# Performance work log

Measured on AMD Instinct MI355X. Metric: run time of the kernel, lower is better.

The kernel has to match this reference:

```python
import jax, jax.numpy as jnp
import numpy as np
import math

N = 512
H = 512
L = 16384
R_MIN, R_MAX, MAX_PHASE = 0.0, 1.0, 6.283


def setup_inputs() -> dict:
    key = jax.random.key(0)
    ks = jax.random.split(key, 8)
    u1 = jax.random.uniform(ks[0], (N,))
    u2 = jax.random.uniform(ks[1], (N,))
    nu_log = jnp.log(-0.5 * jnp.log(u1 * (R_MAX ** 2 - R_MIN ** 2) + R_MIN ** 2))
    theta_log = jnp.log(u2 * MAX_PHASE)
    B_re = jax.random.normal(ks[2], (N, H)) / math.sqrt(2 * H)
    B_im = jax.random.normal(ks[3], (N, H)) / math.sqrt(2 * H)
    C_re = jax.random.normal(ks[4], (H, N)) / math.sqrt(N)
    C_im = jax.random.normal(ks[5], (H, N)) / math.sqrt(N)
    D = jax.random.normal(ks[6], (H,))
    diag_lambda = jnp.exp(-jnp.exp(nu_log) + 1j * jnp.exp(theta_log))
    gamma_log = jnp.log(jnp.sqrt(1.0 - jnp.abs(diag_lambda) ** 2))
    x = jax.random.normal(ks[7], (L, H), dtype=jnp.float32)
    # state is Lambda's multiplier in the original code; ones => standard LRU
    state_re = jnp.ones((N,), dtype=jnp.float32)
    state_im = jnp.zeros((N,), dtype=jnp.float32)
    return {"x": x, "state_re": state_re, "state_im": state_im,
            "nu_log": nu_log, "theta_log": theta_log, "gamma_log": gamma_log,
            "B_re": B_re, "B_im": B_im, "C_re": C_re, "C_im": C_im, "D": D}


def _binop(ei, ej):
    a_i, bu_i = ei
    a_j, bu_j = ej
    return (a_j * a_i, a_j * bu_i + bu_j)


def reference(x, state_re, state_im, nu_log, theta_log, gamma_log,
              B_re, B_im, C_re, C_im, D):
    Lambda = jnp.exp(-jnp.exp(nu_log) + 1j * jnp.exp(theta_log))  # (N,) c64
    # NOTE: original uses exp(i*gamma_log) (a phase), faithful here
    exp_gamma = jnp.exp(1j * gamma_log.astype(jnp.complex64))      # (N,)
    B = (B_re + 1j * B_im) * exp_gamma[:, None]                    # (N,H)
    C = C_re + 1j * C_im                                           # (H,N)
    state = state_re + 1j * state_im                               # (N,)
    a0 = Lambda * state                                            # (N,)
    a_elems = jnp.broadcast_to(a0, (x.shape[0], a0.shape[0]))      # (L,N)
    xc = x.astype(jnp.complex64)                                   # (L,H)
    Bu = xc @ B.T                                                  # (L,N)
    _, inner_states = jax.lax.associative_scan(_binop, (a_elems, Bu))
    y = jnp.real(inner_states @ C.T) + D[None, :] * x              # (L,H)
    return y
```

## Files before the change

kernel.cpp:

```cpp
#include <hip/hip_runtime.h>
#include <hip/hip_bf16.h>
#include <cstdint>

#define L_SEQ 16384
#define NST   512
#define HDIM  512
#define CH    512
#define CT    32

typedef __attribute__((ext_vector_type(8))) short short8;
typedef __attribute__((ext_vector_type(4))) float f32x4;

static __device__ __forceinline__ ushort f2bf(float f) {
  union { float f; unsigned int u; } v; v.f = f;
  unsigned int r = v.u + 0x7fffu + ((v.u >> 16) & 1u);
  return (ushort)(r >> 16);
}
static __device__ __forceinline__ float bf2f(ushort u) {
  union { unsigned int u; float f; } v; v.u = ((unsigned int)u) << 16;
  return v.f;
}

static __device__ __forceinline__ void mfma_16x16x32_bf16(f32x4& d, short8 a, short8 b) {
  asm("v_mfma_f32_16x16x32_bf16 %0, %1, %2, %0" : "+v"(d) : "v"(a), "v"(b));
}

static __device__ __forceinline__ void gload_lds16(const ushort* g, ushort* l) {
  __builtin_amdgcn_global_load_lds((__attribute__((address_space(1))) void*)(g),
                                   (__attribute__((address_space(3))) void*)(l),
                                   16, 0, 0);
}

__global__ __launch_bounds__(256) void setup_kernel(
    const float* __restrict__ st_re, const float* __restrict__ st_im,
    const float* __restrict__ nu_log, const float* __restrict__ theta_log,
    const float* __restrict__ gamma_log,
    const float* __restrict__ B_re, const float* __restrict__ B_im,
    const float* __restrict__ C_re, const float* __restrict__ C_im,
    float2* __restrict__ lam, float2* __restrict__ lamT,
    ushort* __restrict__ W1, ushort* __restrict__ W2)
{
  int bid = blockIdx.x, tid = threadIdx.x;
  if (bid < 1024) {
    int idx = bid * 256 + tid;
    int n = idx >> 9, h = idx & 511;
    float g = gamma_log[n];
    float sg, cg; sincosf(g, &sg, &cg);
    float br = B_re[idx], bi = B_im[idx];
    W1[(size_t)n * 512 + h]         = f2bf(br * cg - bi * sg);
    W1[(size_t)(n + 512) * 512 + h] = f2bf(br * sg + bi * cg);
  } else if (bid < 2048) {
    int idx = (bid - 1024) * 256 + tid;
    int hh = idx >> 9, n = idx & 511;
    W2[(size_t)hh * 1024 + n]       = f2bf(C_re[idx]);
    W2[(size_t)hh * 1024 + 512 + n] = f2bf(-C_im[idx]);
  } else {
    int n = (bid - 2048) * 256 + tid;
    float nu  = expf(nu_log[n]);
    float th  = expf(theta_log[n]);
    float mag = expf(-nu);
    float sth, cth; sincosf(th, &sth, &cth);
    float lr = mag * cth, li = mag * sth;
    float sr = st_re[n], si = st_im[n];
    float ar = lr * sr - li * si;
    float ai = lr * si + li * sr;
    lam[n] = make_float2(ar, ai);
    float pr = ar, pi = ai;
#pragma unroll
    for (int i = 0; i < 5; ++i) {
      float nr = pr * pr - pi * pi;
      float ni = 2.f * pr * pi;
      pr = nr; pi = ni;
    }
    lamT[n] = make_float2(pr, pi);
  }
}

__global__ __launch_bounds__(256) void castX(const float* __restrict__ X,
                                             ushort* __restrict__ xb)
{
  size_t i = ((size_t)blockIdx.x * 256 + threadIdx.x) * 8;
#pragma unroll
  for (int j = 0; j < 8; j += 4) {
    float4 v = *(const float4*)(X + i + j);
    ushort4 o;
    o.x = f2bf(v.x); o.y = f2bf(v.y); o.z = f2bf(v.z); o.w = f2bf(v.w);
    *(ushort4*)(xb + i + j) = o;
  }
}

template <int BM, int BN, int WMW, int WNW, int EPI>
__global__ __launch_bounds__(WMW * WNW * 64, 2)
void gemm_p(const ushort* __restrict__ A, const ushort* __restrict__ Bm,
            ushort* __restrict__ Cb, float* __restrict__ Cf,
            const float* __restrict__ Dv, const float* __restrict__ X,
            int M, int Ncols, int K)
{
  constexpr int THREADS = WMW * WNW * 64;
  constexpr int FM = BM / (WMW * 16);
  constexpr int FN = BN / (WNW * 16);
  constexpr int SLOT = (BM + BN) * 32;
  constexpr int GR = (BM + BN) * 4;
  constexpr int LPT = GR / THREADS;
  static_assert(LPT == 4, "vmcnt immediates assume 4 loads/thread/tile");
  __shared__ __align__(16) ushort lds[4 * SLOT];

  const int t = threadIdx.x, lane = t & 63, w = t >> 6;
  const int wr = w / WNW, wc = w % WNW;
  const int m0 = blockIdx.x * BM, n0 = blockIdx.y * BN;
  const int rr = lane & 15, kk = (lane >> 4) * 8;
  const int NK = K / 32;

  f32x4 acc[FM][FN];
#pragma unroll
  for (int i = 0; i < FM; ++i)
#pragma unroll
    for (int j = 0; j < FN; ++j) { f32x4 z = {0.f, 0.f, 0.f, 0.f}; acc[i][j] = z; }

  auto stage = [&](int kt) {
    int k0 = kt * 32;
    ushort* base = lds + (kt & 3) * SLOT;
#pragma unroll
    for (int j = 0; j < LPT; ++j) {
      int d = j * THREADS + t;
      const ushort* g;
      if (d < BM * 4) g = A  + (size_t)(m0 + (d >> 2)) * K + k0 + (d & 3) * 8;
      else { int dd = d - BM * 4;
             g = Bm + (size_t)(n0 + (dd >> 2)) * K + k0 + (dd & 3) * 8; }
      gload_lds16(g, base + d * 8);
    }
  };

  stage(0); stage(1); stage(2);
  asm volatile("s_waitcnt vmcnt(8)" ::: "memory");
  asm volatile("s_barrier" ::: "memory");

  for (int kt = 0; kt < NK; ++kt) {
    const ushort* As = lds + (kt & 3) * SLOT;
    const ushort* Bs = As + BM * 32;
    short8 af[FM], bb[FN];
#pragma unroll
    for (int mi = 0; mi < FM; ++mi)
      af[mi] = *(const short8*)(As + (wr * FM * 16 + mi * 16 + rr) * 32 + kk);
#pragma unroll
    for (int ni = 0; ni < FN; ++ni)
      bb[ni] = *(const short8*)(Bs + (wc * FN * 16 + ni * 16 + rr) * 32 + kk);
    if (kt + 3 < NK) stage(kt + 3);
    asm volatile("s_waitcnt lgkmcnt(0)" ::: "memory");
    __builtin_amdgcn_sched_barrier(0);
    __builtin_amdgcn_s_setprio(1);
#pragma unroll
    for (int mi = 0; mi < FM; ++mi)
#pragma unroll
      for (int ni = 0; ni < FN; ++ni)
        mfma_16x16x32_bf16(acc[mi][ni], af[mi], bb[ni]);
    __builtin_amdgcn_s_setprio(0);
    __builtin_amdgcn_sched_barrier(0);
    if (kt < NK - 3)       asm volatile("s_waitcnt vmcnt(8)" ::: "memory");
    else if (kt == NK - 3) asm volatile("s_waitcnt vmcnt(4)" ::: "memory");
    else                   asm volatile("s_waitcnt vmcnt(0)" ::: "memory");
    asm volatile("s_barrier" ::: "memory");
  }

  const int crow = (lane >> 4) * 4, ccol = lane & 15;
#pragma unroll
  for (int mi = 0; mi < FM; ++mi) {
#pragma unroll
    for (int ni = 0; ni < FN; ++ni) {
      int col = n0 + wc * FN * 16 + ni * 16 + ccol;
#pragma unroll
      for (int r = 0; r < 4; ++r) {
        int row = m0 + wr * FM * 16 + mi * 16 + crow + r;
        float v = acc[mi][ni][r];
        size_t idx = (size_t)row * Ncols + col;
        if (EPI == 0) Cb[idx] = f2bf(v);
        else          Cf[idx] = v + Dv[col] * X[idx];
      }
    }
  }
}

__global__ __launch_bounds__(256) void scanA(const ushort* __restrict__ Bu,
                                             const float2* __restrict__ lam,
                                             float2* __restrict__ carry)
{
  int q = threadIdx.x;
  int c = blockIdx.x;
  float2 a0 = lam[2 * q], a1 = lam[2 * q + 1];
  float cr0 = 0.f, ci0 = 0.f, cr1 = 0.f, ci1 = 0.f;
  const ushort* base = Bu + (size_t)c * CT * 1024 + 2 * q;
#pragma unroll 4
  for (int tt = 0; tt < CT; ++tt) {
    ushort2 re = *(const ushort2*)(base + tt * 1024);
    ushort2 im = *(const ushort2*)(base + tt * 1024 + 512);
    float br0 = bf2f(re.x), br1 = bf2f(re.y);
    float bi0 = bf2f(im.x), bi1 = bf2f(im.y);
    float nr0 = a0.x * cr0 - a0.y * ci0 + br0;
    float ni0 = a0.x * ci0 + a0.y * cr0 + bi0;
    cr0 = nr0; ci0 = ni0;
    float nr1 = a1.x * cr1 - a1.y * ci1 + br1;
    float ni1 = a1.x * ci1 + a1.y * cr1 + bi1;
    cr1 = nr1; ci1 = ni1;
  }
  carry[(size_t)(2 * q) * CH + c]     = make_float2(cr0, ci0);
  carry[(size_t)(2 * q + 1) * CH + c] = make_float2(cr1, ci1);
}

__global__ __launch_bounds__(CH) void scanC(const float2* __restrict__ carry,
                                            const float2* __restrict__ lamT,
                                            float2* __restrict__ prefix)
{
  int n = blockIdx.x;
  int c = threadIdx.x;
  __shared__ float2 buf[CH];
  float2 aT = lamT[n];
  float2 v = carry[(size_t)n * CH + c];
  buf[c] = v;
  __syncthreads();
  float mr = aT.x, mi = aT.y;
#pragma unroll
  for (int s = 1; s < CH; s <<= 1) {
    float2 o = make_float2(0.f, 0.f);
    if (c >= s) o = buf[c - s];
    __syncthreads();
    v.x += mr * o.x - mi * o.y;
    v.y += mr * o.y + mi * o.x;
    buf[c] = v;
    __syncthreads();
    float nmr = mr * mr - mi * mi;
    float nmi = 2.f * mr * mi;
    mr = nmr; mi = nmi;
  }
  float2 p = (c == 0) ? make_float2(0.f, 0.f) : buf[c - 1];
  prefix[(size_t)n * CH + c] = p;
}

__global__ __launch_bounds__(256) void scanB(ushort* __restrict__ Bu,
                                             const float2* __restrict__ lam,
                                             const float2* __restrict__ prefix)
{
  int q = threadIdx.x;
  int c = blockIdx.x;
  float2 a0 = lam[2 * q], a1 = lam[2 * q + 1];
  float2 g0 = prefix[(size_t)(2 * q) * CH + c];
  float2 g1 = prefix[(size_t)(2 * q + 1) * CH + c];
  float hr0 = g0.x, hi0 = g0.y, hr1 = g1.x, hi1 = g1.y;
  ushort* base = Bu + (size_t)c * CT * 1024 + 2 * q;
#pragma unroll 4
  for (int tt = 0; tt < CT; ++tt) {
    ushort2 re = *(const ushort2*)(base + tt * 1024);
    ushort2 im = *(const ushort2*)(base + tt * 1024 + 512);
    float nr0 = a0.x * hr0 - a0.y * hi0 + bf2f(re.x);
    float ni0 = a0.x * hi0 + a0.y * hr0 + bf2f(im.x);
    hr0 = nr0; hi0 = ni0;
    float nr1 = a1.x * hr1 - a1.y * hi1 + bf2f(re.y);
    float ni1 = a1.x * hi1 + a1.y * hr1 + bf2f(im.y);
    hr1 = nr1; hi1 = ni1;
    ushort2 ore, oim;
    ore.x = f2bf(hr0); ore.y = f2bf(hr1);
    oim.x = f2bf(hi0); oim.y = f2bf(hi1);
    *(ushort2*)(base + tt * 1024)       = ore;
    *(ushort2*)(base + tt * 1024 + 512) = oim;
  }
}

extern "C" void kernel_launch(void* const* d_in, const int* in_sizes, int n_in,
                              void* d_out, int out_size, void* d_ws, size_t ws_size,
                              hipStream_t stream)
{
  const float* x         = (const float*)d_in[0];
  const float* state_re  = (const float*)d_in[1];
  const float* state_im  = (const float*)d_in[2];
  const float* nu_log    = (const float*)d_in[3];
  const float* theta_log = (const float*)d_in[4];
  const float* gamma_log = (const float*)d_in[5];
  const float* B_re      = (const float*)d_in[6];
  const float* B_im      = (const float*)d_in[7];
  const float* C_re      = (const float*)d_in[8];
  const float* C_im      = (const float*)d_in[9];
  const float* Dv        = (const float*)d_in[10];
  float* y = (float*)d_out;

  char* ws = (char*)d_ws;
  size_t off = 0;
  float2* lam    = (float2*)(ws + off); off += 4096;
  float2* lamT   = (float2*)(ws + off); off += 4096;
  float2* carry  = (float2*)(ws + off); off += (size_t)CH * NST * sizeof(float2);
  float2* prefix = (float2*)(ws + off); off += (size_t)CH * NST * sizeof(float2);
  ushort* W1 = (ushort*)(ws + off); off += (size_t)2 * NST * HDIM * sizeof(ushort);
  ushort* W2 = (ushort*)(ws + off); off += (size_t)HDIM * 2 * NST * sizeof(ushort);
  ushort* xb = (ushort*)(ws + off); off += (size_t)L_SEQ * HDIM * sizeof(ushort);
  ushort* Bu = (ushort*)(ws + off); off += (size_t)L_SEQ * 2 * NST * sizeof(ushort);

  setup_kernel<<<2050, 256, 0, stream>>>(state_re, state_im, nu_log, theta_log,
                                         gamma_log, B_re, B_im, C_re, C_im,
                                         lam, lamT, W1, W2);
  castX<<<(L_SEQ * HDIM) / (256 * 8), 256, 0, stream>>>(x, xb);

  gemm_p<256, 256, 2, 4, 0><<<dim3(L_SEQ / 256, (2 * NST) / 256), 512, 0, stream>>>(
      xb, W1, Bu, nullptr, nullptr, nullptr, L_SEQ, 2 * NST, HDIM);

  scanA<<<CH, 256, 0, stream>>>(Bu, lam, carry);
  scanC<<<NST, CH, 0, stream>>>(carry, lamT, prefix);
  scanB<<<CH, 256, 0, stream>>>(Bu, lam, prefix);

  gemm_p<128, 128, 2, 2, 1><<<dim3(L_SEQ / 128, HDIM / 128), 256, 0, stream>>>(
      Bu, W2, nullptr, y, Dv, x, L_SEQ, HDIM, 2 * NST);
}
```

Measured before the change: 93.79 us.

## Swizzle GEMM LDS tiles to avoid bank conflicts and merge cast into setup

Applies an XOR swizzle to the 16-byte k-slot of each row when staging A/B tiles into LDS, and reads them back with a matching swizzle, so the fragment reads in both GEMMs spread across LDS banks instead of conflicting. The castX kernel is folded into the setup kernel as extra blocks, removing one launch. The swizzle must match on both the write and read sides, and it adds a little index arithmetic.

New measurement: 89.92 us. 1.04x faster.

```diff
diff --git a/kernel.cpp b/kernel.cpp
--- a/kernel.cpp
+++ b/kernel.cpp
@@ -31,31 +31,42 @@
                                    16, 0, 0);
 }
 
-__global__ __launch_bounds__(256) void setup_kernel(
+__global__ __launch_bounds__(256) void setup_all(
     const float* __restrict__ st_re, const float* __restrict__ st_im,
     const float* __restrict__ nu_log, const float* __restrict__ theta_log,
     const float* __restrict__ gamma_log,
     const float* __restrict__ B_re, const float* __restrict__ B_im,
     const float* __restrict__ C_re, const float* __restrict__ C_im,
+    const float* __restrict__ X,
     float2* __restrict__ lam, float2* __restrict__ lamT,
-    ushort* __restrict__ W1, ushort* __restrict__ W2)
+    ushort* __restrict__ W1, ushort* __restrict__ W2,
+    ushort* __restrict__ xb)
 {
   int bid = blockIdx.x, tid = threadIdx.x;
-  if (bid < 1024) {
-    int idx = bid * 256 + tid;
+  if (bid < 4096) {
+    size_t i = ((size_t)bid * 256 + tid) * 8;
+#pragma unroll
+    for (int j = 0; j < 8; j += 4) {
+      float4 v = *(const float4*)(X + i + j);
+      ushort4 o;
+      o.x = f2bf(v.x); o.y = f2bf(v.y); o.z = f2bf(v.z); o.w = f2bf(v.w);
+      *(ushort4*)(xb + i + j) = o;
+    }
+  } else if (bid < 5120) {
+    int idx = (bid - 4096) * 256 + tid;
     int n = idx >> 9, h = idx & 511;
     float g = gamma_log[n];
     float sg, cg; sincosf(g, &sg, &cg);
     float br = B_re[idx], bi = B_im[idx];
     W1[(size_t)n * 512 + h]         = f2bf(br * cg - bi * sg);
     W1[(size_t)(n + 512) * 512 + h] = f2bf(br * sg + bi * cg);
-  } else if (bid < 2048) {
-    int idx = (bid - 1024) * 256 + tid;
+  } else if (bid < 6144) {
+    int idx = (bid - 5120) * 256 + tid;
     int hh = idx >> 9, n = idx & 511;
     W2[(size_t)hh * 1024 + n]       = f2bf(C_re[idx]);
     W2[(size_t)hh * 1024 + 512 + n] = f2bf(-C_im[idx]);
   } else {
-    int n = (bid - 2048) * 256 + tid;
+    int n = (bid - 6144) * 256 + tid;
     float nu  = expf(nu_log[n]);
     float th  = expf(theta_log[n]);
     float mag = expf(-nu);
@@ -76,19 +87,6 @@
   }
 }
 
-__global__ __launch_bounds__(256) void castX(const float* __restrict__ X,
-                                             ushort* __restrict__ xb)
-{
-  size_t i = ((size_t)blockIdx.x * 256 + threadIdx.x) * 8;
-#pragma unroll
-  for (int j = 0; j < 8; j += 4) {
-    float4 v = *(const float4*)(X + i + j);
-    ushort4 o;
-    o.x = f2bf(v.x); o.y = f2bf(v.y); o.z = f2bf(v.z); o.w = f2bf(v.w);
-    *(ushort4*)(xb + i + j) = o;
-  }
-}
-
 template <int BM, int BN, int WMW, int WNW, int EPI>
 __global__ __launch_bounds__(WMW * WNW * 64, 2)
 void gemm_p(const ushort* __restrict__ A, const ushort* __restrict__ Bm,
@@ -109,6 +107,7 @@
   const int wr = w / WNW, wc = w % WNW;
   const int m0 = blockIdx.x * BM, n0 = blockIdx.y * BN;
   const int rr = lane & 15, kk = (lane >> 4) * 8;
+  const int swzu = ((rr >> 1) & 3) << 3;
   const int NK = K / 32;
 
   f32x4 acc[FM][FN];
@@ -124,9 +123,16 @@
     for (int j = 0; j < LPT; ++j) {
       int d = j * THREADS + t;
       const ushort* g;
-      if (d < BM * 4) g = A  + (size_t)(m0 + (d >> 2)) * K + k0 + (d & 3) * 8;
-      else { int dd = d - BM * 4;
-             g = Bm + (size_t)(n0 + (dd >> 2)) * K + k0 + (dd & 3) * 8; }
+      if (d < BM * 4) {
+        int row = d >> 2;
+        int sl  = (d & 3) ^ ((row >> 1) & 3);
+        g = A + (size_t)(m0 + row) * K + k0 + sl * 8;
+      } else {
+        int dd = d - BM * 4;
+        int row = dd >> 2;
+        int sl  = (dd & 3) ^ ((row >> 1) & 3);
+        g = Bm + (size_t)(n0 + row) * K + k0 + sl * 8;
+      }
       gload_lds16(g, base + d * 8);
     }
   };
@@ -141,10 +147,10 @@
     short8 af[FM], bb[FN];
 #pragma unroll
     for (int mi = 0; mi < FM; ++mi)
-      af[mi] = *(const short8*)(As + (wr * FM * 16 + mi * 16 + rr) * 32 + kk);
+      af[mi] = *(const short8*)(As + (wr * FM * 16 + mi * 16 + rr) * 32 + (kk ^ swzu));
 #pragma unroll
     for (int ni = 0; ni < FN; ++ni)
-      bb[ni] = *(const short8*)(Bs + (wc * FN * 16 + ni * 16 + rr) * 32 + kk);
+      bb[ni] = *(const short8*)(Bs + (wc * FN * 16 + ni * 16 + rr) * 32 + (kk ^ swzu));
     if (kt + 3 < NK) stage(kt + 3);
     asm volatile("s_waitcnt lgkmcnt(0)" ::: "memory");
     __builtin_amdgcn_sched_barrier(0);
@@ -292,10 +298,9 @@
   ushort* xb = (ushort*)(ws + off); off += (size_t)L_SEQ * HDIM * sizeof(ushort);
   ushort* Bu = (ushort*)(ws + off); off += (size_t)L_SEQ * 2 * NST * sizeof(ushort);
 
-  setup_kernel<<<2050, 256, 0, stream>>>(state_re, state_im, nu_log, theta_log,
-                                         gamma_log, B_re, B_im, C_re, C_im,
-                                         lam, lamT, W1, W2);
-  castX<<<(L_SEQ * HDIM) / (256 * 8), 256, 0, stream>>>(x, xb);
+  setup_all<<<6146, 256, 0, stream>>>(state_re, state_im, nu_log, theta_log,
+                                      gamma_log, B_re, B_im, C_re, C_im, x,
+                                      lam, lamT, W1, W2, xb);
 
   gemm_p<256, 256, 2, 4, 0><<<dim3(L_SEQ / 256, (2 * NST) / 256), 512, 0, stream>>>(
       xb, W1, Bu, nullptr, nullptr, nullptr, L_SEQ, 2 * NST, HDIM);
```
